# Kernel tuning notes

Hardware: AMD Instinct MI355X
Metric: run time of the kernel (lower is better)

## Reference

```python
import jax, jax.numpy as jnp
import numpy as np

D_MODEL = 1024
H = 16
D_K = D_MODEL // H  # 64
RANK = 5
ALPHA = 1.0


def _lora_linear(x, W, b, dW, dB):
    # merged weight: W + alpha * dB @ dW  (shape [out, in]); F.linear -> x @ W_merged.T + b
    Wm = W + ALPHA * (dB @ dW)
    return x @ Wm.T + b


def setup_inputs() -> dict:
    key = jax.random.key(0)
    ks = jax.random.split(key, 16)
    b_s, nq = 2, 2048
    s = 1.0 / np.sqrt(D_MODEL).astype(np.float32)
    inp = {
        "x": jax.random.normal(ks[0], (b_s, nq, D_MODEL), dtype=jnp.float32),
    }
    names = ["q", "k", "v", "o"]
    i = 1
    for n in names:
        inp[f"{n}_w"] = jax.random.normal(ks[i], (D_MODEL, D_MODEL), dtype=jnp.float32) * s; i += 1
        inp[f"{n}_b"] = jnp.zeros((D_MODEL,), dtype=jnp.float32)
        inp[f"{n}_dw"] = jax.random.normal(ks[i], (RANK, D_MODEL), dtype=jnp.float32) * 0.01; i += 1
        inp[f"{n}_db"] = jax.random.normal(ks[i], (D_MODEL, RANK), dtype=jnp.float32) * 0.01; i += 1
    return inp


def reference(x, q_w, q_b, q_dw, q_db, k_w, k_b, k_dw, k_db,
              v_w, v_b, v_dw, v_db, o_w, o_b, o_dw, o_db):
    b_s, nq, _ = x.shape
    q = _lora_linear(x, q_w, q_b, q_dw, q_db).reshape(b_s, nq, H, D_K)
    k = _lora_linear(x, k_w, k_b, k_dw, k_db).reshape(b_s, nq, H, D_K)
    v = _lora_linear(x, v_w, v_b, v_dw, v_db).reshape(b_s, nq, H, D_K)
    # scores: [b, h, q, k]
    att = jnp.einsum("bqhd,bkhd->bhqk", q, k) / np.sqrt(D_K).astype(np.float32)
    att = jax.nn.softmax(att, axis=-1)
    out = jnp.einsum("bhqk,bkhd->bqhd", att, v).reshape(b_s, nq, H * D_K)
    out = _lora_linear(out, o_w, o_b, o_dw, o_db)
    return out
```

## Files before the change

### kernel.cpp

```cpp
#include <hip/hip_runtime.h>
#include <hip/hip_bf16.h>

#define NQ 2048
#define NB 2

typedef unsigned short u16;
typedef unsigned int u32;
typedef _Float16 f16;
typedef __attribute__((ext_vector_type(8))) _Float16 half8;
typedef __attribute__((ext_vector_type(2))) __fp16 fp16x2;
typedef __attribute__((ext_vector_type(4))) float f32x4;

#define MFMAH(A, B, C) __builtin_amdgcn_mfma_f32_16x16x32_f16(A, B, C, 0, 0, 0)

__device__ __forceinline__ u16 f2h(float x) {
    f16 h = (f16)x;
    return *(u16*)&h;
}
__device__ __forceinline__ u32 pk_h2(float a, float b) {
    union { fp16x2 v; u32 u; } c;
    c.v = __builtin_amdgcn_cvt_pkrtz(a, b);
    return c.u;
}
__device__ __forceinline__ float fexp2(float x) {
#if __has_builtin(__builtin_amdgcn_exp2f)
    return __builtin_amdgcn_exp2f(x);
#else
    return exp2f(x);
#endif
}
__device__ __forceinline__ void glds16(const u16* g, u16* l) {
    typedef const __attribute__((address_space(1))) u16 gu16;
    typedef __attribute__((address_space(3))) u16 lu16;
    __builtin_amdgcn_global_load_lds((gu16*)g, (lu16*)l, 16, 0, 0);
}

#define QSCALE 0.18033688011112042f

__global__ __launch_bounds__(256) void merge_w16(
    const float* __restrict__ w0, const float* __restrict__ dw0, const float* __restrict__ db0,
    const float* __restrict__ w1, const float* __restrict__ dw1, const float* __restrict__ db1,
    const float* __restrict__ w2, const float* __restrict__ dw2, const float* __restrict__ db2,
    const float* __restrict__ w3, const float* __restrict__ dw3, const float* __restrict__ db3,
    u16* __restrict__ Wf) {
    int idx = blockIdx.x * 256 + threadIdx.x;
    int row = idx >> 10, col = idx & 1023;
    int which = row >> 10, lr = row & 1023;
    const float* W  = (which == 0) ? w0  : (which == 1) ? w1  : (which == 2) ? w2  : w3;
    const float* dW = (which == 0) ? dw0 : (which == 1) ? dw1 : (which == 2) ? dw2 : dw3;
    const float* dB = (which == 0) ? db0 : (which == 1) ? db1 : (which == 2) ? db2 : db3;
    float acc = W[lr * 1024 + col];
#pragma unroll
    for (int r = 0; r < 5; ++r) acc += dB[lr * 5 + r] * dW[r * 1024 + col];
    if (which == 0) acc *= QSCALE;
    Wf[idx] = f2h(acc);
}

__global__ __launch_bounds__(256) void bias_pack(
    const float* __restrict__ b0, const float* __restrict__ b1,
    const float* __restrict__ b2, const float* __restrict__ b3,
    float* __restrict__ ball) {
    int t = blockIdx.x * 256 + threadIdx.x;
    int which = t >> 10;
    const float* B = (which == 0) ? b0 : (which == 1) ? b1 : (which == 2) ? b2 : b3;
    float v = B[t & 1023];
    if (which == 0) v *= QSCALE;
    ball[t] = v;
}

__global__ __launch_bounds__(256) void xcast(const float* __restrict__ x,
                                             u16* __restrict__ xf) {
    int i4 = (blockIdx.x * 256 + threadIdx.x) * 4;
    float4 v = *(const float4*)&x[i4];
    *(uint2*)&xf[i4] = make_uint2(pk_h2(v.x, v.y), pk_h2(v.z, v.w));
}

template <int TM>
__global__ __launch_bounds__(256) void gemm_f16(
    const u16* __restrict__ Af, const u16* __restrict__ Bf,
    const float* __restrict__ bias,
    float* __restrict__ Cf, u16* __restrict__ Cb, int ldc,
    u16* __restrict__ VtOut) {
    constexpr int MI = TM / 32;
    __shared__ u16 As[2][TM * 32];
    __shared__ u16 Bs[2][128 * 32];
    const int tid = threadIdx.x;
    const int wid = tid >> 6, lane = tid & 63;
    const int ln = lane & 15, quad = lane >> 4;
    const int bm = blockIdx.y * TM, bn = blockIdx.x * 128;
    const int wm = (wid >> 1) * (TM / 2), wn = (wid & 1) * 64;
    const int lrow = lane >> 2;
    const int lchunk = (lane & 3) * 8;

    f32x4 acc[MI][4];
#pragma unroll
    for (int i = 0; i < MI; ++i)
#pragma unroll
        for (int j = 0; j < 4; ++j) acc[i][j] = (f32x4){0.f, 0.f, 0.f, 0.f};

    for (int k0 = 0; k0 < 1024; k0 += 64) {
#pragma unroll
        for (int hf = 0; hf < 2; ++hf) {
#pragma unroll
            for (int p = 0; p < TM / 64; ++p) {
                int r = p * 64 + wid * 16;
                glds16(&Af[(bm + r + lrow) * 1024 + k0 + hf * 32 + lchunk],
                       &As[hf][r * 32]);
            }
#pragma unroll
            for (int p = 0; p < 2; ++p) {
                int r = p * 64 + wid * 16;
                glds16(&Bf[(bn + r + lrow) * 1024 + k0 + hf * 32 + lchunk],
                       &Bs[hf][r * 32]);
            }
        }
        asm volatile("s_waitcnt vmcnt(0)" ::: "memory");
        __syncthreads();

        half8 a[MI][2], b[4][2];
#pragma unroll
        for (int kc = 0; kc < 2; ++kc) {
#pragma unroll
            for (int j = 0; j < 4; ++j)
                b[j][kc] = *(const half8*)&Bs[kc][(wn + j * 16 + ln) * 32 + quad * 8];
#pragma unroll
            for (int i = 0; i < MI; ++i)
                a[i][kc] = *(const half8*)&As[kc][(wm + i * 16 + ln) * 32 + quad * 8];
        }
#pragma unroll
        for (int i = 0; i < MI; ++i)
#pragma unroll
            for (int j = 0; j < 4; ++j) {
                acc[i][j] = MFMAH(a[i][0], b[j][0], acc[i][j]);
                acc[i][j] = MFMAH(a[i][1], b[j][1], acc[i][j]);
            }
        __syncthreads();
    }

    if (VtOut && bn >= 2048) {
#pragma unroll
        for (int i = 0; i < MI; ++i)
#pragma unroll
            for (int j = 0; j < 4; ++j) {
                int col = bn + wn + j * 16 + ln;
                float bv = bias[col];
                int colV = col - 2048;
                int row0 = bm + wm + i * 16 + quad * 4;
                ushort4 pk = make_ushort4(f2h(acc[i][j][0] + bv), f2h(acc[i][j][1] + bv),
                                          f2h(acc[i][j][2] + bv), f2h(acc[i][j][3] + bv));
                *(ushort4*)&VtOut[colV * 4096 + row0] = pk;
            }
        return;
    }

#pragma unroll
    for (int i = 0; i < MI; ++i)
#pragma unroll
        for (int j = 0; j < 4; ++j) {
            int col = bn + wn + j * 16 + ln;
            float bv = bias[col];
#pragma unroll
            for (int r = 0; r < 4; ++r) {
                int row = bm + wm + i * 16 + quad * 4 + r;
                float v = acc[i][j][r] + bv;
                if (Cb) Cb[row * ldc + col] = f2h(v);
                else    Cf[row * ldc + col] = v;
            }
        }
}

__global__ __launch_bounds__(256) void flash_f16(
    const u16* __restrict__ QKV, const u16* __restrict__ Vt,
    u16* __restrict__ AO) {
    __shared__ u16 Ks[2][64 * 72];
    __shared__ u16 Vs[2][64 * 72];
    __shared__ u16 Ps[4][32 * 64];

    const int tid = threadIdx.x;
    const int wid = tid >> 6, lane = tid & 63;
    const int ln = lane & 15, quad = lane >> 4;
    const int qt = blockIdx.x, h = blockIdx.y, b = blockIdx.z;
    const int rowbase = b * NQ;
    const int col0 = h * 64;
    const int q0 = rowbase + qt * 128 + wid * 32;

    const half8 ones = {(f16)1, (f16)1, (f16)1, (f16)1,
                        (f16)1, (f16)1, (f16)1, (f16)1};

    half8 qf[2][2];
#pragma unroll
    for (int mi = 0; mi < 2; ++mi)
#pragma unroll
        for (int kc = 0; kc < 2; ++kc)
            qf[mi][kc] = *(const half8*)&QKV[(q0 + mi * 16 + ln) * 3072 + col0 +
                                             kc * 32 + quad * 8];

    f32x4 accO[4][2];
    f32x4 accS[2];
#pragma unroll
    for (int mi = 0; mi < 2; ++mi) {
        accS[mi] = (f32x4){0.f, 0.f, 0.f, 0.f};
#pragma unroll
        for (int a = 0; a < 4; ++a) accO[a][mi] = (f32x4){0.f, 0.f, 0.f, 0.f};
    }

    const int srow = tid >> 2;
    const int sc0 = (tid & 3) * 16;
    const int NT = NQ / 64;

    const int swz = ln & 7;

    {
        const u16* kg = QKV + (rowbase + srow) * 3072 + 1024 + col0;
        const u16* vg = Vt + (col0 + srow) * 4096 + rowbase;
        *(uint4*)&Ks[0][srow * 72 + sc0]     = *(const uint4*)&kg[sc0];
        *(uint4*)&Ks[0][srow * 72 + sc0 + 8] = *(const uint4*)&kg[sc0 + 8];
        *(uint4*)&Vs[0][srow * 72 + sc0]     = *(const uint4*)&vg[sc0];
        *(uint4*)&Vs[0][srow * 72 + sc0 + 8] = *(const uint4*)&vg[sc0 + 8];
    }
    __syncthreads();

    for (int kt = 0; kt < NT; ++kt) {
        const int cur = kt & 1;
        uint4 nk0, nk1, nv0, nv1;
        if (kt + 1 < NT) {
            const u16* kg = QKV + (rowbase + (kt + 1) * 64 + srow) * 3072 + 1024 + col0;
            const u16* vg = Vt + (col0 + srow) * 4096 + rowbase + (kt + 1) * 64;
            nk0 = *(const uint4*)&kg[sc0];
            nk1 = *(const uint4*)&kg[sc0 + 8];
            nv0 = *(const uint4*)&vg[sc0];
            nv1 = *(const uint4*)&vg[sc0 + 8];
        }

        f32x4 s[4][2];
#pragma unroll
        for (int a = 0; a < 4; ++a) {
            half8 kf0 = *(const half8*)&Ks[cur][(a * 16 + ln) * 72 + quad * 8];
            half8 kf1 = *(const half8*)&Ks[cur][(a * 16 + ln) * 72 + 32 + quad * 8];
#pragma unroll
            for (int mi = 0; mi < 2; ++mi) {
                f32x4 t = (f32x4){0.f, 0.f, 0.f, 0.f};
                t = MFMAH(kf0, qf[mi][0], t);
                t = MFMAH(kf1, qf[mi][1], t);
                s[a][mi] = t;
            }
        }

#pragma unroll
        for (int mi = 0; mi < 2; ++mi)
#pragma unroll
            for (int a = 0; a < 4; ++a) {
                float p0 = fexp2(s[a][mi][0]), p1 = fexp2(s[a][mi][1]);
                float p2 = fexp2(s[a][mi][2]), p3 = fexp2(s[a][mi][3]);
                uint2 w = make_uint2(pk_h2(p0, p1), pk_h2(p2, p3));
                int chunk = 2 * a + (quad >> 1);
                int addr = (mi * 16 + ln) * 64 + ((chunk ^ swz) << 3) + ((quad & 1) << 2);
                *(uint2*)&Ps[wid][addr] = w;
            }

        asm volatile("s_waitcnt lgkmcnt(0)" ::: "memory");

        half8 pf[2][2];
#pragma unroll
        for (int mi = 0; mi < 2; ++mi)
#pragma unroll
            for (int kc = 0; kc < 2; ++kc) {
                int chunk = kc * 4 + quad;
                pf[mi][kc] = *(const half8*)&Ps[wid][(mi * 16 + ln) * 64 +
                                                     ((chunk ^ swz) << 3)];
                accS[mi] = MFMAH(ones, pf[mi][kc], accS[mi]);
            }

#pragma unroll
        for (int a = 0; a < 4; ++a) {
            half8 vf0 = *(const half8*)&Vs[cur][(a * 16 + ln) * 72 + quad * 8];
            half8 vf1 = *(const half8*)&Vs[cur][(a * 16 + ln) * 72 + 32 + quad * 8];
#pragma unroll
            for (int mi = 0; mi < 2; ++mi) {
                accO[a][mi] = MFMAH(vf0, pf[mi][0], accO[a][mi]);
                accO[a][mi] = MFMAH(vf1, pf[mi][1], accO[a][mi]);
            }
        }

        if (kt + 1 < NT) {
            const int nb = cur ^ 1;
            *(uint4*)&Ks[nb][srow * 72 + sc0]     = nk0;
            *(uint4*)&Ks[nb][srow * 72 + sc0 + 8] = nk1;
            *(uint4*)&Vs[nb][srow * 72 + sc0]     = nv0;
            *(uint4*)&Vs[nb][srow * 72 + sc0 + 8] = nv1;
        }
        __syncthreads();
    }

#pragma unroll
    for (int mi = 0; mi < 2; ++mi) {
        float inv = 1.f / accS[mi][0];
        int q = q0 + mi * 16 + ln;
#pragma unroll
        for (int a = 0; a < 4; ++a) {
            ushort4 pk = make_ushort4(f2h(accO[a][mi][0] * inv),
                                      f2h(accO[a][mi][1] * inv),
                                      f2h(accO[a][mi][2] * inv),
                                      f2h(accO[a][mi][3] * inv));
            *(ushort4*)&AO[q * 1024 + col0 + a * 16 + quad * 4] = pk;
        }
    }
}

extern "C" void kernel_launch(void* const* d_in, const int* in_sizes, int n_in,
                              void* d_out, int out_size, void* d_ws, size_t ws_size,
                              hipStream_t stream) {
    const float* x = (const float*)d_in[0];
    const float* w[4]  = {(const float*)d_in[1],  (const float*)d_in[5],
                          (const float*)d_in[9],  (const float*)d_in[13]};
    const float* bv[4] = {(const float*)d_in[2],  (const float*)d_in[6],
                          (const float*)d_in[10], (const float*)d_in[14]};
    const float* dw[4] = {(const float*)d_in[3],  (const float*)d_in[7],
                          (const float*)d_in[11], (const float*)d_in[15]};
    const float* db[4] = {(const float*)d_in[4],  (const float*)d_in[8],
                          (const float*)d_in[12], (const float*)d_in[16]};

    u16* p = (u16*)d_ws;
    u16* Wf  = p; p += 4096 * 1024;
    u16* xf  = p; p += 4096 * 1024;
    u16* QKV = p; p += 4096 * 3072;
    u16* Vt  = p; p += 1024 * 4096;
    float* ball = (float*)p;
    u16* AO = xf;

    merge_w16<<<16384, 256, 0, stream>>>(w[0], dw[0], db[0], w[1], dw[1], db[1],
                                         w[2], dw[2], db[2], w[3], dw[3], db[3], Wf);
    bias_pack<<<16, 256, 0, stream>>>(bv[0], bv[1], bv[2], bv[3], ball);
    xcast<<<4096, 256, 0, stream>>>(x, xf);

    gemm_f16<128><<<dim3(24, 32), 256, 0, stream>>>(xf, Wf, ball,
                                                    nullptr, QKV, 3072, Vt);

    flash_f16<<<dim3(NQ / 128, 16, NB), 256, 0, stream>>>(QKV, Vt, AO);

    gemm_f16<64><<<dim3(8, 64), 256, 0, stream>>>(AO, Wf + 3072 * 1024,
                                                  ball + 3072, (float*)d_out, nullptr, 1024,
                                                  nullptr);
}
```

Baseline: 225.6 us.

## Split attention KV range in two and combine partial outputs

Each flash block now handles only half of the key/value sequence, which doubles the grid to raise CU occupancy and parallelism. Unnormalized partial outputs are written in fp16, and the partial softmax denominators in fp32. A new combine kernel sums the two halves and normalizes them. This adds an extra global round trip for the partial outputs plus one more kernel launch. Storing unnormalized partials in fp16 risks some precision loss.

```diff
diff --git a/kernel.cpp b/kernel.cpp
--- a/kernel.cpp
+++ b/kernel.cpp
@@ -28,6 +28,10 @@
 #else
     return exp2f(x);
 #endif
+}
+__device__ __forceinline__ float h2f(u16 u) {
+    f16 h = *(f16*)&u;
+    return (float)h;
 }
 __device__ __forceinline__ void glds16(const u16* g, u16* l) {
     typedef const __attribute__((address_space(1))) u16 gu16;
@@ -171,7 +175,7 @@
 
 __global__ __launch_bounds__(256) void flash_f16(
     const u16* __restrict__ QKV, const u16* __restrict__ Vt,
-    u16* __restrict__ AO) {
+    u16* __restrict__ Opart, float* __restrict__ Spart) {
     __shared__ u16 Ks[2][64 * 72];
     __shared__ u16 Vs[2][64 * 72];
     __shared__ u16 Ps[4][32 * 64];
@@ -179,7 +183,8 @@
     const int tid = threadIdx.x;
     const int wid = tid >> 6, lane = tid & 63;
     const int ln = lane & 15, quad = lane >> 4;
-    const int qt = blockIdx.x, h = blockIdx.y, b = blockIdx.z;
+    const int qt = blockIdx.x, h = blockIdx.y;
+    const int b = blockIdx.z >> 1, kh = blockIdx.z & 1;
     const int rowbase = b * NQ;
     const int col0 = h * 64;
     const int q0 = rowbase + qt * 128 + wid * 32;
@@ -206,13 +211,12 @@
 
     const int srow = tid >> 2;
     const int sc0 = (tid & 3) * 16;
-    const int NT = NQ / 64;
-
+    const int kt0 = kh * 16, kt1 = kt0 + 16;
     const int swz = ln & 7;
 
     {
-        const u16* kg = QKV + (rowbase + srow) * 3072 + 1024 + col0;
-        const u16* vg = Vt + (col0 + srow) * 4096 + rowbase;
+        const u16* kg = QKV + (rowbase + kt0 * 64 + srow) * 3072 + 1024 + col0;
+        const u16* vg = Vt + (col0 + srow) * 4096 + rowbase + kt0 * 64;
         *(uint4*)&Ks[0][srow * 72 + sc0]     = *(const uint4*)&kg[sc0];
         *(uint4*)&Ks[0][srow * 72 + sc0 + 8] = *(const uint4*)&kg[sc0 + 8];
         *(uint4*)&Vs[0][srow * 72 + sc0]     = *(const uint4*)&vg[sc0];
@@ -220,10 +224,10 @@
     }
     __syncthreads();
 
-    for (int kt = 0; kt < NT; ++kt) {
+    for (int kt = kt0; kt < kt1; ++kt) {
         const int cur = kt & 1;
         uint4 nk0, nk1, nv0, nv1;
-        if (kt + 1 < NT) {
+        if (kt + 1 < kt1) {
             const u16* kg = QKV + (rowbase + (kt + 1) * 64 + srow) * 3072 + 1024 + col0;
             const u16* vg = Vt + (col0 + srow) * 4096 + rowbase + (kt + 1) * 64;
             nk0 = *(const uint4*)&kg[sc0];
@@ -282,7 +286,7 @@
             }
         }
 
-        if (kt + 1 < NT) {
+        if (kt + 1 < kt1) {
             const int nb = cur ^ 1;
             *(uint4*)&Ks[nb][srow * 72 + sc0]     = nk0;
             *(uint4*)&Ks[nb][srow * 72 + sc0 + 8] = nk1;
@@ -294,17 +298,34 @@
 
 #pragma unroll
     for (int mi = 0; mi < 2; ++mi) {
-        float inv = 1.f / accS[mi][0];
         int q = q0 + mi * 16 + ln;
 #pragma unroll
         for (int a = 0; a < 4; ++a) {
-            ushort4 pk = make_ushort4(f2h(accO[a][mi][0] * inv),
-                                      f2h(accO[a][mi][1] * inv),
-                                      f2h(accO[a][mi][2] * inv),
-                                      f2h(accO[a][mi][3] * inv));
-            *(ushort4*)&AO[q * 1024 + col0 + a * 16 + quad * 4] = pk;
-        }
-    }
+            ushort4 pk = make_ushort4(f2h(accO[a][mi][0]), f2h(accO[a][mi][1]),
+                                      f2h(accO[a][mi][2]), f2h(accO[a][mi][3]));
+            *(ushort4*)&Opart[(size_t)kh * 4096 * 1024 + q * 1024 + col0 +
+                              a * 16 + quad * 4] = pk;
+        }
+        if (quad == 0) Spart[kh * 4096 * 16 + q * 16 + h] = accS[mi][0];
+    }
+}
+
+__global__ __launch_bounds__(256) void combine(
+    const u16* __restrict__ Opart, const float* __restrict__ Spart,
+    u16* __restrict__ AO) {
+    int idx = blockIdx.x * 256 + threadIdx.x;
+    int row = idx >> 8;
+    int c0 = (idx & 255) * 4;
+    int h = c0 >> 6;
+    float s = Spart[row * 16 + h] + Spart[4096 * 16 + row * 16 + h];
+    float inv = 1.f / s;
+    ushort4 o0 = *(const ushort4*)&Opart[(size_t)row * 1024 + c0];
+    ushort4 o1 = *(const ushort4*)&Opart[(size_t)4096 * 1024 + row * 1024 + c0];
+    ushort4 pk = make_ushort4(f2h((h2f(o0.x) + h2f(o1.x)) * inv),
+                              f2h((h2f(o0.y) + h2f(o1.y)) * inv),
+                              f2h((h2f(o0.z) + h2f(o1.z)) * inv),
+                              f2h((h2f(o0.w) + h2f(o1.w)) * inv));
+    *(ushort4*)&AO[(size_t)row * 1024 + c0] = pk;
 }
 
 extern "C" void kernel_launch(void* const* d_in, const int* in_sizes, int n_in,
@@ -321,11 +342,13 @@
                           (const float*)d_in[12], (const float*)d_in[16]};
 
     u16* p = (u16*)d_ws;
-    u16* Wf  = p; p += 4096 * 1024;
-    u16* xf  = p; p += 4096 * 1024;
-    u16* QKV = p; p += 4096 * 3072;
-    u16* Vt  = p; p += 1024 * 4096;
-    float* ball = (float*)p;
+    u16* Wf    = p; p += 4096 * 1024;
+    u16* xf    = p; p += 4096 * 1024;
+    u16* QKV   = p; p += 4096 * 3072;
+    u16* Vt    = p; p += 1024 * 4096;
+    u16* Opart = p; p += 2 * 4096 * 1024;
+    float* Spart = (float*)p; p += 2 * 4096 * 16 * 2;
+    float* ball  = (float*)p;
     u16* AO = xf;
 
     merge_w16<<<16384, 256, 0, stream>>>(w[0], dw[0], db[0], w[1], dw[1], db[1],
@@ -336,7 +359,8 @@
     gemm_f16<128><<<dim3(24, 32), 256, 0, stream>>>(xf, Wf, ball,
                                                     nullptr, QKV, 3072, Vt);
 
-    flash_f16<<<dim3(NQ / 128, 16, NB), 256, 0, stream>>>(QKV, Vt, AO);
+    flash_f16<<<dim3(NQ / 128, 16, NB * 2), 256, 0, stream>>>(QKV, Vt, Opart, Spart);
+    combine<<<4096, 256, 0, stream>>>(Opart, Spart, AO);
 
     gemm_f16<64><<<dim3(8, 64), 256, 0, stream>>>(AO, Wf + 3072 * 1024,
                                                   ball + 3072, (float*)d_out, nullptr, 1024,
```

Result: slower. 237.3 us (+5.2%).

## Halve flash attention query tile per block and vectorize LoRA weight merge

Applied to the files above, without the earlier changes.

The flash kernel now handles 64 queries per block (16 per wave) instead of 128, doubling the grid to 1024 blocks so more CUs are busy and register pressure per wave drops. In exchange, K/V tiles are loaded from global memory twice as often relative to compute, and each K/V LDS fragment feeds fewer MFMAs. Separately, the weight merge kernel processes four columns per thread with float4 loads and packed fp16 stores, cutting its launch size to a quarter.

```diff
diff --git a/kernel.cpp b/kernel.cpp
--- a/kernel.cpp
+++ b/kernel.cpp
@@ -43,17 +43,23 @@
     const float* __restrict__ w2, const float* __restrict__ dw2, const float* __restrict__ db2,
     const float* __restrict__ w3, const float* __restrict__ dw3, const float* __restrict__ db3,
     u16* __restrict__ Wf) {
-    int idx = blockIdx.x * 256 + threadIdx.x;
-    int row = idx >> 10, col = idx & 1023;
+    int t = blockIdx.x * 256 + threadIdx.x;
+    int row = t >> 8, c4 = (t & 255) << 2;
     int which = row >> 10, lr = row & 1023;
     const float* W  = (which == 0) ? w0  : (which == 1) ? w1  : (which == 2) ? w2  : w3;
     const float* dW = (which == 0) ? dw0 : (which == 1) ? dw1 : (which == 2) ? dw2 : dw3;
     const float* dB = (which == 0) ? db0 : (which == 1) ? db1 : (which == 2) ? db2 : db3;
-    float acc = W[lr * 1024 + col];
-#pragma unroll
-    for (int r = 0; r < 5; ++r) acc += dB[lr * 5 + r] * dW[r * 1024 + col];
-    if (which == 0) acc *= QSCALE;
-    Wf[idx] = f2h(acc);
+    float4 acc = *(const float4*)&W[lr * 1024 + c4];
+#pragma unroll
+    for (int r = 0; r < 5; ++r) {
+        float b = dB[lr * 5 + r];
+        float4 d = *(const float4*)&dW[r * 1024 + c4];
+        acc.x += b * d.x; acc.y += b * d.y; acc.z += b * d.z; acc.w += b * d.w;
+    }
+    if (which == 0) {
+        acc.x *= QSCALE; acc.y *= QSCALE; acc.z *= QSCALE; acc.w *= QSCALE;
+    }
+    *(uint2*)&Wf[row * 1024 + c4] = make_uint2(pk_h2(acc.x, acc.y), pk_h2(acc.z, acc.w));
 }
 
 __global__ __launch_bounds__(256) void bias_pack(
@@ -174,7 +180,7 @@
     u16* __restrict__ AO) {
     __shared__ u16 Ks[2][64 * 72];
     __shared__ u16 Vs[2][64 * 72];
-    __shared__ u16 Ps[4][32 * 64];
+    __shared__ u16 Ps[4][16 * 64];
 
     const int tid = threadIdx.x;
     const int wid = tid >> 6, lane = tid & 63;
@@ -182,32 +188,24 @@
     const int qt = blockIdx.x, h = blockIdx.y, b = blockIdx.z;
     const int rowbase = b * NQ;
     const int col0 = h * 64;
-    const int q0 = rowbase + qt * 128 + wid * 32;
+    const int q0 = rowbase + qt * 64 + wid * 16;
 
     const half8 ones = {(f16)1, (f16)1, (f16)1, (f16)1,
                         (f16)1, (f16)1, (f16)1, (f16)1};
 
-    half8 qf[2][2];
-#pragma unroll
-    for (int mi = 0; mi < 2; ++mi)
-#pragma unroll
-        for (int kc = 0; kc < 2; ++kc)
-            qf[mi][kc] = *(const half8*)&QKV[(q0 + mi * 16 + ln) * 3072 + col0 +
-                                             kc * 32 + quad * 8];
-
-    f32x4 accO[4][2];
-    f32x4 accS[2];
-#pragma unroll
-    for (int mi = 0; mi < 2; ++mi) {
-        accS[mi] = (f32x4){0.f, 0.f, 0.f, 0.f};
-#pragma unroll
-        for (int a = 0; a < 4; ++a) accO[a][mi] = (f32x4){0.f, 0.f, 0.f, 0.f};
-    }
+    half8 qf[2];
+#pragma unroll
+    for (int kc = 0; kc < 2; ++kc)
+        qf[kc] = *(const half8*)&QKV[(q0 + ln) * 3072 + col0 + kc * 32 + quad * 8];
+
+    f32x4 accO[4];
+    f32x4 accS = (f32x4){0.f, 0.f, 0.f, 0.f};
+#pragma unroll
+    for (int a = 0; a < 4; ++a) accO[a] = (f32x4){0.f, 0.f, 0.f, 0.f};
 
     const int srow = tid >> 2;
     const int sc0 = (tid & 3) * 16;
     const int NT = NQ / 64;
-
     const int swz = ln & 7;
 
     {
@@ -232,54 +230,43 @@
             nv1 = *(const uint4*)&vg[sc0 + 8];
         }
 
-        f32x4 s[4][2];
+        f32x4 s[4];
 #pragma unroll
         for (int a = 0; a < 4; ++a) {
             half8 kf0 = *(const half8*)&Ks[cur][(a * 16 + ln) * 72 + quad * 8];
             half8 kf1 = *(const half8*)&Ks[cur][(a * 16 + ln) * 72 + 32 + quad * 8];
-#pragma unroll
-            for (int mi = 0; mi < 2; ++mi) {
-                f32x4 t = (f32x4){0.f, 0.f, 0.f, 0.f};
-                t = MFMAH(kf0, qf[mi][0], t);
-                t = MFMAH(kf1, qf[mi][1], t);
-                s[a][mi] = t;
-            }
-        }
-
-#pragma unroll
-        for (int mi = 0; mi < 2; ++mi)
-#pragma unroll
-            for (int a = 0; a < 4; ++a) {
-                float p0 = fexp2(s[a][mi][0]), p1 = fexp2(s[a][mi][1]);
-                float p2 = fexp2(s[a][mi][2]), p3 = fexp2(s[a][mi][3]);
-                uint2 w = make_uint2(pk_h2(p0, p1), pk_h2(p2, p3));
-                int chunk = 2 * a + (quad >> 1);
-                int addr = (mi * 16 + ln) * 64 + ((chunk ^ swz) << 3) + ((quad & 1) << 2);
-                *(uint2*)&Ps[wid][addr] = w;
-            }
+            f32x4 t = (f32x4){0.f, 0.f, 0.f, 0.f};
+            t = MFMAH(kf0, qf[0], t);
+            t = MFMAH(kf1, qf[1], t);
+            s[a] = t;
+        }
+
+#pragma unroll
+        for (int a = 0; a < 4; ++a) {
+            float p0 = fexp2(s[a][0]), p1 = fexp2(s[a][1]);
+            float p2 = fexp2(s[a][2]), p3 = fexp2(s[a][3]);
+            uint2 w = make_uint2(pk_h2(p0, p1), pk_h2(p2, p3));
+            int chunk = 2 * a + (quad >> 1);
+            int addr = ln * 64 + ((chunk ^ swz) << 3) + ((quad & 1) << 2);
+            *(uint2*)&Ps[wid][addr] = w;
+        }
 
         asm volatile("s_waitcnt lgkmcnt(0)" ::: "memory");
 
-        half8 pf[2][2];
-#pragma unroll
-        for (int mi = 0; mi < 2; ++mi)
-#pragma unroll
-            for (int kc = 0; kc < 2; ++kc) {
-                int chunk = kc * 4 + quad;
-                pf[mi][kc] = *(const half8*)&Ps[wid][(mi * 16 + ln) * 64 +
-                                                     ((chunk ^ swz) << 3)];
-                accS[mi] = MFMAH(ones, pf[mi][kc], accS[mi]);
-            }
+        half8 pf[2];
+#pragma unroll
+        for (int kc = 0; kc < 2; ++kc) {
+            int chunk = kc * 4 + quad;
+            pf[kc] = *(const half8*)&Ps[wid][ln * 64 + ((chunk ^ swz) << 3)];
+            accS = MFMAH(ones, pf[kc], accS);
+        }
 
 #pragma unroll
         for (int a = 0; a < 4; ++a) {
             half8 vf0 = *(const half8*)&Vs[cur][(a * 16 + ln) * 72 + quad * 8];
             half8 vf1 = *(const half8*)&Vs[cur][(a * 16 + ln) * 72 + 32 + quad * 8];
-#pragma unroll
-            for (int mi = 0; mi < 2; ++mi) {
-                accO[a][mi] = MFMAH(vf0, pf[mi][0], accO[a][mi]);
-                accO[a][mi] = MFMAH(vf1, pf[mi][1], accO[a][mi]);
-            }
+            accO[a] = MFMAH(vf0, pf[0], accO[a]);
+            accO[a] = MFMAH(vf1, pf[1], accO[a]);
         }
 
         if (kt + 1 < NT) {
@@ -292,16 +279,15 @@
         __syncthreads();
     }
 
-#pragma unroll
-    for (int mi = 0; mi < 2; ++mi) {
-        float inv = 1.f / accS[mi][0];
-        int q = q0 + mi * 16 + ln;
+    {
+        float inv = 1.f / accS[0];
+        int q = q0 + ln;
 #pragma unroll
         for (int a = 0; a < 4; ++a) {
-            ushort4 pk = make_ushort4(f2h(accO[a][mi][0] * inv),
-                                      f2h(accO[a][mi][1] * inv),
-                                      f2h(accO[a][mi][2] * inv),
-                                      f2h(accO[a][mi][3] * inv));
+            ushort4 pk = make_ushort4(f2h(accO[a][0] * inv),
+                                      f2h(accO[a][1] * inv),
+                                      f2h(accO[a][2] * inv),
+                                      f2h(accO[a][3] * inv));
             *(ushort4*)&AO[q * 1024 + col0 + a * 16 + quad * 4] = pk;
         }
     }
@@ -328,15 +314,15 @@
     float* ball = (float*)p;
     u16* AO = xf;
 
-    merge_w16<<<16384, 256, 0, stream>>>(w[0], dw[0], db[0], w[1], dw[1], db[1],
-                                         w[2], dw[2], db[2], w[3], dw[3], db[3], Wf);
+    merge_w16<<<4096, 256, 0, stream>>>(w[0], dw[0], db[0], w[1], dw[1], db[1],
+                                        w[2], dw[2], db[2], w[3], dw[3], db[3], Wf);
     bias_pack<<<16, 256, 0, stream>>>(bv[0], bv[1], bv[2], bv[3], ball);
     xcast<<<4096, 256, 0, stream>>>(x, xf);
 
     gemm_f16<128><<<dim3(24, 32), 256, 0, stream>>>(xf, Wf, ball,
                                                     nullptr, QKV, 3072, Vt);
 
-    flash_f16<<<dim3(NQ / 128, 16, NB), 256, 0, stream>>>(QKV, Vt, AO);
+    flash_f16<<<dim3(NQ / 64, 16, NB), 256, 0, stream>>>(QKV, Vt, AO);
 
     gemm_f16<64><<<dim3(8, 64), 256, 0, stream>>>(AO, Wf + 3072 * 1024,
                                                   ball + 3072, (float*)d_out, nullptr, 1024,
```

Result: slower. 240.6 us (+6.6%).
